# Optimization experiments

Hardware: AMD Instinct MI355X
Metric: run time of the kernel (lower is better)

## Reference

```python
import jax, jax.numpy as jnp
import numpy as np

NEG_BIG = -9e15
ALPHA = 0.2  # LeakyReLU negative slope


def setup_inputs() -> dict:
    key = jax.random.key(0)
    k1, k2, k3, k4 = jax.random.split(key, 4)
    N, Fin, Fout = 8192, 256, 256
    input_ = jax.random.normal(k1, (N, Fin), dtype=jnp.float32)
    adj = jax.random.randint(k2, (N, N), 0, 2, dtype=jnp.int32)
    # xavier_uniform with gain=1.414
    limW = 1.414 * np.sqrt(6.0 / (Fin + Fout))
    W = jax.random.uniform(k3, (Fin, Fout), minval=-limW, maxval=limW, dtype=jnp.float32)
    lima = 1.414 * np.sqrt(6.0 / (2 * Fout + 1))
    a = jax.random.uniform(k4, (2 * Fout, 1), minval=-lima, maxval=lima, dtype=jnp.float32)
    return {"input_": input_, "adj": adj, "W": W, "a": a}


def reference(input_, adj, W, a):
    # h: [N, F]
    h = input_ @ W
    F = h.shape[1]
    # Decompose cat([h_i, h_j]) @ a into per-node projections summed by broadcast
    src = h @ a[:F, 0]   # [N]  contribution of row node i
    dst = h @ a[F:, 0]   # [N]  contribution of col node j
    e = jax.nn.leaky_relu(src[:, None] + dst[None, :], negative_slope=ALPHA)  # [N, N]
    e = jnp.where(adj > 0, e, NEG_BIG)
    attention = jax.nn.softmax(e, axis=1)
    h_prime = attention @ h  # [N, F]
    return jax.nn.relu(h_prime)  # concat=True
```

## Files before the change

kernel.cpp:

```cpp
#include <hip/hip_runtime.h>
#include <math.h>

#define NN 8192
#define FF 256
#define ALPHA 0.2f
#define SS 8
#define JSEG (NN / SS)
#define STEPS (JSEG / 32)

typedef __bf16 bf16x8 __attribute__((ext_vector_type(8)));
typedef __bf16 bf16x4 __attribute__((ext_vector_type(4)));
typedef float  f32x4  __attribute__((ext_vector_type(4)));

__device__ __forceinline__ void dma16(const void* g, void* l) {
    __builtin_amdgcn_global_load_lds((const __attribute__((address_space(1))) void*)g,
                                     (__attribute__((address_space(3))) void*)l,
                                     16, 0, 0);
}

#define VMCNT0   asm volatile("s_waitcnt vmcnt(0)" ::: "memory")
#define LGKM0    asm volatile("s_waitcnt lgkmcnt(0)" ::: "memory")
#define BARRIER  asm volatile("s_barrier" ::: "memory")
#define FENCE    asm volatile("" ::: "memory")

__global__ __launch_bounds__(256) void k0_wt(const float* __restrict__ W,
                                             __bf16* __restrict__ WT) {
    __shared__ float ts[64][65];
    const int t = threadIdx.x;
    const int k0 = blockIdx.x * 64;
    const int n0 = blockIdx.y * 64;
    #pragma unroll
    for (int r = 0; r < 4; ++r) {
        int krow = r * 16 + (t >> 4);
        int nc4 = (t & 15) * 4;
        *(float4*)&ts[krow][nc4] = *(const float4*)&W[(size_t)(k0 + krow) * FF + n0 + nc4];
    }
    __syncthreads();
    const int nloc = t >> 2;
    const int kc = (t & 3) * 16;
    union { bf16x8 v[2]; __bf16 e[16]; } hi, lo;
    #pragma unroll
    for (int u = 0; u < 16; ++u) {
        float x = ts[kc + u][nloc];
        __bf16 h1 = (__bf16)x;
        hi.e[u] = h1;
        lo.e[u] = (__bf16)(x - (float)h1);
    }
    size_t base = (size_t)(n0 + nloc) * FF + k0 + kc;
    *(bf16x8*)&WT[base] = hi.v[0];
    *(bf16x8*)&WT[base + 8] = hi.v[1];
    size_t lbase = (size_t)FF * FF + base;
    *(bf16x8*)&WT[lbase] = lo.v[0];
    *(bf16x8*)&WT[lbase + 8] = lo.v[1];
}

__global__ __launch_bounds__(256) void k1_h(const float* __restrict__ X,
                                            const __bf16* __restrict__ WT,
                                            const float* __restrict__ a,
                                            __bf16* __restrict__ hT,
                                            float* __restrict__ src,
                                            float* __restrict__ dst) {
    __shared__ __bf16 ax[2][32][40];
    __shared__ float hs[32][264];
    __shared__ float red[2][4][32];
    const int t = threadIdx.x;
    const int i0 = blockIdx.x * 32;
    const int l = t & 63, wv = t >> 6, ln = l & 15, g = l >> 4;
    f32x4 acc[2][4];
    #pragma unroll
    for (int mt = 0; mt < 2; ++mt)
        #pragma unroll
        for (int nt = 0; nt < 4; ++nt)
            acc[mt][nt] = (f32x4){0.f, 0.f, 0.f, 0.f};

    for (int ks = 0; ks < 8; ++ks) {
        const int k0 = ks * 32;
        {
            int row = t >> 3, c4 = (t & 7) * 4;
            float4 xv = *(const float4*)&X[(size_t)(i0 + row) * FF + k0 + c4];
            bf16x4 hi4, lo4;
            float xs_[4] = {xv.x, xv.y, xv.z, xv.w};
            #pragma unroll
            for (int u = 0; u < 4; ++u) {
                __bf16 h1 = (__bf16)xs_[u];
                hi4[u] = h1;
                lo4[u] = (__bf16)(xs_[u] - (float)h1);
            }
            *(bf16x4*)&ax[0][row][c4] = hi4;
            *(bf16x4*)&ax[1][row][c4] = lo4;
        }
        __syncthreads();
        bf16x8 ah[2], al[2];
        ah[0] = *(bf16x8*)&ax[0][ln][g * 8];
        ah[1] = *(bf16x8*)&ax[0][16 + ln][g * 8];
        al[0] = *(bf16x8*)&ax[1][ln][g * 8];
        al[1] = *(bf16x8*)&ax[1][16 + ln][g * 8];
        #pragma unroll
        for (int nt = 0; nt < 4; ++nt) {
            const int n = wv * 64 + nt * 16 + ln;
            bf16x8 bh8 = *(const bf16x8*)&WT[(size_t)n * FF + k0 + g * 8];
            bf16x8 bl8 = *(const bf16x8*)&WT[(size_t)(FF + n) * FF + k0 + g * 8];
            #pragma unroll
            for (int mt = 0; mt < 2; ++mt) {
                acc[mt][nt] = __builtin_amdgcn_mfma_f32_16x16x32_bf16(ah[mt], bh8, acc[mt][nt], 0, 0, 0);
                acc[mt][nt] = __builtin_amdgcn_mfma_f32_16x16x32_bf16(ah[mt], bl8, acc[mt][nt], 0, 0, 0);
                acc[mt][nt] = __builtin_amdgcn_mfma_f32_16x16x32_bf16(al[mt], bh8, acc[mt][nt], 0, 0, 0);
            }
        }
        __syncthreads();
    }
    float an[4], ad[4];
    #pragma unroll
    for (int nt = 0; nt < 4; ++nt) {
        an[nt] = a[wv * 64 + nt * 16 + ln];
        ad[nt] = a[FF + wv * 64 + nt * 16 + ln];
    }
    float sp[2][4], dp[2][4];
    #pragma unroll
    for (int mt = 0; mt < 2; ++mt)
        #pragma unroll
        for (int rg = 0; rg < 4; ++rg) { sp[mt][rg] = 0.f; dp[mt][rg] = 0.f; }
    #pragma unroll
    for (int mt = 0; mt < 2; ++mt)
        #pragma unroll
        for (int nt = 0; nt < 4; ++nt)
            #pragma unroll
            for (int rg = 0; rg < 4; ++rg) {
                float v = acc[mt][nt][rg];
                hs[mt * 16 + g * 4 + rg][wv * 64 + nt * 16 + ln] = v;
                sp[mt][rg] += v * an[nt];
                dp[mt][rg] += v * ad[nt];
            }
    #pragma unroll
    for (int mk = 1; mk < 16; mk <<= 1)
        #pragma unroll
        for (int mt = 0; mt < 2; ++mt)
            #pragma unroll
            for (int rg = 0; rg < 4; ++rg) {
                sp[mt][rg] += __shfl_xor(sp[mt][rg], mk);
                dp[mt][rg] += __shfl_xor(dp[mt][rg], mk);
            }
    if (ln == 0) {
        #pragma unroll
        for (int mt = 0; mt < 2; ++mt)
            #pragma unroll
            for (int rg = 0; rg < 4; ++rg) {
                red[0][wv][mt * 16 + g * 4 + rg] = sp[mt][rg];
                red[1][wv][mt * 16 + g * 4 + rg] = dp[mt][rg];
            }
    }
    __syncthreads();
    if (t < 32) {
        src[i0 + t] = red[0][0][t] + red[0][1][t] + red[0][2][t] + red[0][3][t];
        dst[i0 + t] = red[1][0][t] + red[1][1][t] + red[1][2][t] + red[1][3][t];
    }
    {
        const int f = t;
        #pragma unroll
        for (int jc = 0; jc < 4; ++jc) {
            union { bf16x8 v; __bf16 e[8]; } hi;
            #pragma unroll
            for (int u = 0; u < 8; ++u) {
                float x = hs[jc * 8 + u][f];
                hi.e[u] = (__bf16)x;
            }
            *(bf16x8*)&hT[(size_t)f * NN + i0 + jc * 8] = hi.v;
        }
    }
}

__global__ __launch_bounds__(256) void k2a_pack(const int* __restrict__ adj,
                                                unsigned* __restrict__ bits) {
    const size_t total4 = (size_t)NN * NN / 4;
    const int l = threadIdx.x & 63;
    const int base = l & 56;
    size_t t = (size_t)blockIdx.x * 256 + threadIdx.x;
    const size_t stride = (size_t)gridDim.x * 256;
    for (; t < total4; t += stride) {
        int4 v = ((const int4*)adj)[t];
        unsigned nib = (unsigned)(v.x > 0) | ((unsigned)(v.y > 0) << 1)
                     | ((unsigned)(v.z > 0) << 2) | ((unsigned)(v.w > 0) << 3);
        unsigned w = 0;
        #pragma unroll
        for (int k = 0; k < 8; ++k)
            w |= (unsigned)__shfl((int)nib, base + k) << (4 * k);
        if ((l & 7) == 0)
            bits[t >> 3] = w;
    }
}

__global__ __launch_bounds__(256) void k2b_max(const float* __restrict__ dst,
                                               float* __restrict__ maxd) {
    __shared__ float red[256];
    float m = -1e30f;
    #pragma unroll
    for (int r = 0; r < NN / 1024; ++r) {
        float4 v = *(const float4*)&dst[(r * 256 + threadIdx.x) * 4];
        m = fmaxf(m, fmaxf(fmaxf(v.x, v.y), fmaxf(v.z, v.w)));
    }
    red[threadIdx.x] = m;
    __syncthreads();
    for (int s = 128; s > 0; s >>= 1) {
        if (threadIdx.x < s) red[threadIdx.x] = fmaxf(red[threadIdx.x], red[threadIdx.x + s]);
        __syncthreads();
    }
    if (threadIdx.x == 0) maxd[0] = red[0];
}

__global__ __launch_bounds__(256, 4) void k3_attn(const unsigned* __restrict__ bits,
                                                  const __bf16* __restrict__ hT,
                                                  const float* __restrict__ src,
                                                  const float* __restrict__ dst,
                                                  const float* __restrict__ maxd,
                                                  float* __restrict__ num,
                                                  float* __restrict__ den) {
    __shared__ __bf16 bh[2][1024 * 8];
    __shared__ float dsts[JSEG];
    const int t = threadIdx.x;
    const int l = t & 63, wv = t >> 6, ln = l & 15, g = l >> 4;
    const int it = blockIdx.x & 127;
    const int seg = blockIdx.x >> 7;
    const int i0 = it * 64;
    const int jbeg = seg * JSEG;
    const int rl = wv * 16 + ln;
    const int row = i0 + rl;
    const float maxdv = maxd[0];
    const float src_r = src[row];
    const float e0 = src_r + maxdv;
    const float m_r = e0 > 0.f ? e0 : ALPHA * e0;

    int ga[4], cb[4];
    #pragma unroll
    for (int r = 0; r < 4; ++r) {
        int cbase = r * 256 + wv * 64;
        int c = cbase + l;
        int f = c >> 2;
        int pc = c & 3;
        int jc = pc ^ ((f >> 1) & 3);
        ga[r] = f * NN + jc * 8;
        cb[r] = __builtin_amdgcn_readfirstlane(cbase);
    }
    const int rb = ln * 64 + ((g ^ ((ln >> 1) & 3)) * 16);
    const char* bh0 = (const char*)&bh[0][0] + rb;
    const char* bh1 = (const char*)&bh[1][0] + rb;

    const unsigned* grow = bits + (size_t)row * (NN / 32) + (jbeg >> 5);

    #pragma unroll
    for (int r = 0; r < 4; ++r)
        dma16(&hT[ga[r] + jbeg], &bh[0][cb[r] * 8]);
    FENCE;
    *(float4*)&dsts[t * 4] = *(const float4*)&dst[jbeg + t * 4];
    uint2 wp = *(const uint2*)&grow[0];
    uint2 wpn = wp;
    __syncthreads();

    float den_reg = 0.f;
    f32x4 acc[16];
    #pragma unroll
    for (int nt = 0; nt < 16; ++nt) acc[nt] = (f32x4){0.f, 0.f, 0.f, 0.f};

#define K3_WCOMP(S_, MW_, AF_)                                                \
    {                                                                         \
        unsigned mb = ((MW_) >> (g * 8)) & 0xffu;                             \
        const float* dp_ = &dsts[(S_) * 32 + g * 8];                          \
        float4 dq0 = *(const float4*)dp_;                                     \
        float4 dq1 = *(const float4*)(dp_ + 4);                               \
        const float dv[8] = {dq0.x, dq0.y, dq0.z, dq0.w,                      \
                             dq1.x, dq1.y, dq1.z, dq1.w};                     \
        _Pragma("unroll")                                                     \
        for (int u = 0; u < 8; ++u) {                                         \
            float e = src_r + dv[u];                                          \
            e = e > 0.f ? e : ALPHA * e;                                      \
            float ex = __expf(e - m_r);                                       \
            float w = (mb & (1u << u)) ? ex : 0.f;                            \
            den_reg += w;                                                     \
            AF_.e[u] = (__bf16)w;                                             \
        }                                                                     \
    }

#define K3_MFMA(AF_, BP_)                                                     \
    {                                                                         \
        _Pragma("unroll")                                                     \
        for (int nt = 0; nt < 16; ++nt) {                                     \
            bf16x8 bfr = *(const bf16x8*)((BP_) + nt * 1024);                 \
            acc[nt] = __builtin_amdgcn_mfma_f32_16x16x32_bf16(                \
                AF_.v, bfr, acc[nt], 0, 0, 0);                                \
        }                                                                     \
    }

    for (int s = 0; s < STEPS; s += 2) {
        union { bf16x8 v; __bf16 e[8]; } afe;
        K3_WCOMP(s, wp.x, afe);
        FENCE; VMCNT0; LGKM0; BARRIER;
        #pragma unroll
        for (int r = 0; r < 4; ++r)
            dma16(&hT[ga[r] + jbeg + (s + 1) * 32], &bh[1][cb[r] * 8]);
        if (s + 2 < STEPS) wpn = *(const uint2*)&grow[s + 2];
        FENCE;
        K3_MFMA(afe, bh0);
        union { bf16x8 v; __bf16 e[8]; } afo;
        K3_WCOMP(s + 1, wp.y, afo);
        FENCE; VMCNT0; LGKM0; BARRIER;
        {
            int sn = (s + 2 < STEPS) ? s + 2 : 0;
            #pragma unroll
            for (int r = 0; r < 4; ++r)
                dma16(&hT[ga[r] + jbeg + sn * 32], &bh[0][cb[r] * 8]);
        }
        FENCE;
        K3_MFMA(afo, bh1);
        wp = wpn;
    }
    den_reg += __shfl_xor(den_reg, 16);
    den_reg += __shfl_xor(den_reg, 32);
    if (g == 0) den[(size_t)seg * NN + row] = den_reg;
    #pragma unroll
    for (int nt = 0; nt < 16; ++nt)
        #pragma unroll
        for (int rg = 0; rg < 4; ++rg)
            num[((size_t)seg * NN + i0 + wv * 16 + g * 4 + rg) * FF
                + nt * 16 + ln] = acc[nt][rg];
}

__global__ __launch_bounds__(256) void k4_out(const float* __restrict__ num,
                                              const float* __restrict__ den,
                                              float* __restrict__ out) {
    size_t f4 = (size_t)blockIdx.x * 256 + threadIdx.x;
    int i = (int)(f4 >> 6);
    int c4 = (int)(f4 & 63) << 2;
    float4 s = make_float4(0.f, 0.f, 0.f, 0.f);
    float d = 0.f;
    #pragma unroll
    for (int sg = 0; sg < SS; ++sg) {
        float4 v = *(const float4*)&num[((size_t)sg * NN + i) * FF + c4];
        s.x += v.x; s.y += v.y; s.z += v.z; s.w += v.w;
        d += den[(size_t)sg * NN + i];
    }
    float inv = 1.f / d;
    float4 o;
    o.x = fmaxf(s.x * inv, 0.f);
    o.y = fmaxf(s.y * inv, 0.f);
    o.z = fmaxf(s.z * inv, 0.f);
    o.w = fmaxf(s.w * inv, 0.f);
    *(float4*)&out[(size_t)i * FF + c4] = o;
}

extern "C" void kernel_launch(void* const* d_in, const int* in_sizes, int n_in,
                              void* d_out, int out_size, void* d_ws, size_t ws_size,
                              hipStream_t stream) {
    const float* X  = (const float*)d_in[0];
    const int*  adj = (const int*)d_in[1];
    const float* W  = (const float*)d_in[2];
    const float* a  = (const float*)d_in[3];
    float* out = (float*)d_out;
    char* ws = (char*)d_ws;

    const size_t off_hT   = 0;
    const size_t off_wt   = off_hT + (size_t)FF * NN * 2;
    const size_t off_src  = off_wt + (size_t)2 * FF * FF * 2;
    const size_t off_dst  = off_src + (size_t)NN * 4;
    const size_t off_maxd = off_dst + (size_t)NN * 4;
    const size_t off_num  = off_maxd + 256;
    const size_t off_den  = off_num + (size_t)SS * NN * FF * 4;
    const size_t off_bits = off_den + (size_t)SS * NN * 4;

    __bf16* hT_ws = (__bf16*)(ws + off_hT);
    __bf16* wt_ws = (__bf16*)(ws + off_wt);
    float* src_ws = (float*)(ws + off_src);
    float* dst_ws = (float*)(ws + off_dst);
    float* maxd   = (float*)(ws + off_maxd);
    float* num_ws = (float*)(ws + off_num);
    float* den_ws = (float*)(ws + off_den);
    unsigned* bits_ws = (unsigned*)(ws + off_bits);

    k2a_pack<<<2048, 256, 0, stream>>>(adj, bits_ws);
    k0_wt<<<dim3(FF / 64, FF / 64), 256, 0, stream>>>(W, wt_ws);
    k1_h<<<NN / 32, 256, 0, stream>>>(X, wt_ws, a, hT_ws, src_ws, dst_ws);
    k2b_max<<<1, 256, 0, stream>>>(dst_ws, maxd);
    k3_attn<<<(NN / 64) * SS, 256, 0, stream>>>(bits_ws, hT_ws, src_ws, dst_ws, maxd,
                                                num_ws, den_ws);
    k4_out<<<(NN * FF / 4) / 256, 256, 0, stream>>>(num_ws, den_ws, out);
}
```

Baseline: 455.4 us.

## Switch attention kernel to 32x32x16 MFMA with 128-row tiles

After: 456.0 us. About the same (+0.1%).

```diff
diff --git a/kernel.cpp b/kernel.cpp
--- a/kernel.cpp
+++ b/kernel.cpp
@@ -7,10 +7,12 @@
 #define SS 8
 #define JSEG (NN / SS)
 #define STEPS (JSEG / 32)
+#define BI 128
 
 typedef __bf16 bf16x8 __attribute__((ext_vector_type(8)));
 typedef __bf16 bf16x4 __attribute__((ext_vector_type(4)));
 typedef float  f32x4  __attribute__((ext_vector_type(4)));
+typedef float  f32x16 __attribute__((ext_vector_type(16)));
 
 __device__ __forceinline__ void dma16(const void* g, void* l) {
     __builtin_amdgcn_global_load_lds((const __attribute__((address_space(1))) void*)g,
@@ -207,7 +209,7 @@
     if (threadIdx.x == 0) maxd[0] = red[0];
 }
 
-__global__ __launch_bounds__(256, 4) void k3_attn(const unsigned* __restrict__ bits,
+__global__ __launch_bounds__(256, 2) void k3_attn(const unsigned* __restrict__ bits,
                                                   const __bf16* __restrict__ hT,
                                                   const float* __restrict__ src,
                                                   const float* __restrict__ dst,
@@ -217,13 +219,13 @@
     __shared__ __bf16 bh[2][1024 * 8];
     __shared__ float dsts[JSEG];
     const int t = threadIdx.x;
-    const int l = t & 63, wv = t >> 6, ln = l & 15, g = l >> 4;
-    const int it = blockIdx.x & 127;
-    const int seg = blockIdx.x >> 7;
-    const int i0 = it * 64;
+    const int l = t & 63, wv = t >> 6;
+    const int q = l & 31, hi = l >> 5;
+    const int it = blockIdx.x & 63;
+    const int seg = blockIdx.x >> 6;
+    const int i0 = it * BI;
     const int jbeg = seg * JSEG;
-    const int rl = wv * 16 + ln;
-    const int row = i0 + rl;
+    const int row = i0 + wv * 32 + q;
     const float maxdv = maxd[0];
     const float src_r = src[row];
     const float e0 = src_r + maxdv;
@@ -236,13 +238,14 @@
         int c = cbase + l;
         int f = c >> 2;
         int pc = c & 3;
-        int jc = pc ^ ((f >> 1) & 3);
+        int jc = pc ^ (f & 3);
         ga[r] = f * NN + jc * 8;
         cb[r] = __builtin_amdgcn_readfirstlane(cbase);
     }
-    const int rb = ln * 64 + ((g ^ ((ln >> 1) & 3)) * 16);
-    const char* bh0 = (const char*)&bh[0][0] + rb;
-    const char* bh1 = (const char*)&bh[1][0] + rb;
+    const int rb0 = q * 64 + (((0 + hi) ^ (q & 3)) * 16);
+    const int rb1 = q * 64 + (((2 + hi) ^ (q & 3)) * 16);
+    const char* bh0 = (const char*)&bh[0][0];
+    const char* bh1 = (const char*)&bh[1][0];
 
     const unsigned* grow = bits + (size_t)row * (NN / 32) + (jbeg >> 5);
 
@@ -256,51 +259,68 @@
     __syncthreads();
 
     float den_reg = 0.f;
-    f32x4 acc[16];
-    #pragma unroll
-    for (int nt = 0; nt < 16; ++nt) acc[nt] = (f32x4){0.f, 0.f, 0.f, 0.f};
-
-#define K3_WCOMP(S_, MW_, AF_)                                                \
+    f32x16 acc[8];
+    #pragma unroll
+    for (int ft = 0; ft < 8; ++ft)
+        #pragma unroll
+        for (int rg = 0; rg < 16; ++rg) acc[ft][rg] = 0.f;
+
+#define K3_WCOMP(S_, MW_, AF0_, AF1_)                                         \
     {                                                                         \
-        unsigned mb = ((MW_) >> (g * 8)) & 0xffu;                             \
-        const float* dp_ = &dsts[(S_) * 32 + g * 8];                          \
-        float4 dq0 = *(const float4*)dp_;                                     \
-        float4 dq1 = *(const float4*)(dp_ + 4);                               \
-        const float dv[8] = {dq0.x, dq0.y, dq0.z, dq0.w,                      \
-                             dq1.x, dq1.y, dq1.z, dq1.w};                     \
+        unsigned mb0 = ((MW_) >> (hi * 8)) & 0xffu;                           \
+        unsigned mb1 = ((MW_) >> (16 + hi * 8)) & 0xffu;                      \
+        const float* dp0 = &dsts[(S_) * 32 + hi * 8];                         \
+        float4 a0 = *(const float4*)dp0;                                      \
+        float4 a1 = *(const float4*)(dp0 + 4);                                \
+        float4 b0 = *(const float4*)(dp0 + 16);                               \
+        float4 b1 = *(const float4*)(dp0 + 20);                               \
+        const float dv0[8] = {a0.x, a0.y, a0.z, a0.w, a1.x, a1.y, a1.z, a1.w};\
+        const float dv1[8] = {b0.x, b0.y, b0.z, b0.w, b1.x, b1.y, b1.z, b1.w};\
         _Pragma("unroll")                                                     \
         for (int u = 0; u < 8; ++u) {                                         \
-            float e = src_r + dv[u];                                          \
+            float e = src_r + dv0[u];                                         \
             e = e > 0.f ? e : ALPHA * e;                                      \
             float ex = __expf(e - m_r);                                       \
-            float w = (mb & (1u << u)) ? ex : 0.f;                            \
+            float w = (mb0 & (1u << u)) ? ex : 0.f;                           \
             den_reg += w;                                                     \
-            AF_.e[u] = (__bf16)w;                                             \
+            AF0_.e[u] = (__bf16)w;                                            \
         }                                                                     \
-    }
-
-#define K3_MFMA(AF_, BP_)                                                     \
+        _Pragma("unroll")                                                     \
+        for (int u = 0; u < 8; ++u) {                                         \
+            float e = src_r + dv1[u];                                         \
+            e = e > 0.f ? e : ALPHA * e;                                      \
+            float ex = __expf(e - m_r);                                       \
+            float w = (mb1 & (1u << u)) ? ex : 0.f;                           \
+            den_reg += w;                                                     \
+            AF1_.e[u] = (__bf16)w;                                            \
+        }                                                                     \
+    }
+
+#define K3_MFMA(AF0_, AF1_, BP_)                                              \
     {                                                                         \
         _Pragma("unroll")                                                     \
-        for (int nt = 0; nt < 16; ++nt) {                                     \
-            bf16x8 bfr = *(const bf16x8*)((BP_) + nt * 1024);                 \
-            acc[nt] = __builtin_amdgcn_mfma_f32_16x16x32_bf16(                \
-                AF_.v, bfr, acc[nt], 0, 0, 0);                                \
+        for (int ft = 0; ft < 8; ++ft) {                                      \
+            bf16x8 bk0 = *(const bf16x8*)((BP_) + ft * 2048 + rb0);           \
+            bf16x8 bk1 = *(const bf16x8*)((BP_) + ft * 2048 + rb1);           \
+            acc[ft] = __builtin_amdgcn_mfma_f32_32x32x16_bf16(                \
+                AF0_.v, bk0, acc[ft], 0, 0, 0);                               \
+            acc[ft] = __builtin_amdgcn_mfma_f32_32x32x16_bf16(                \
+                AF1_.v, bk1, acc[ft], 0, 0, 0);                               \
         }                                                                     \
     }
 
     for (int s = 0; s < STEPS; s += 2) {
-        union { bf16x8 v; __bf16 e[8]; } afe;
-        K3_WCOMP(s, wp.x, afe);
+        union { bf16x8 v; __bf16 e[8]; } af0e, af1e;
+        K3_WCOMP(s, wp.x, af0e, af1e);
         FENCE; VMCNT0; LGKM0; BARRIER;
         #pragma unroll
         for (int r = 0; r < 4; ++r)
             dma16(&hT[ga[r] + jbeg + (s + 1) * 32], &bh[1][cb[r] * 8]);
         if (s + 2 < STEPS) wpn = *(const uint2*)&grow[s + 2];
         FENCE;
-        K3_MFMA(afe, bh0);
-        union { bf16x8 v; __bf16 e[8]; } afo;
-        K3_WCOMP(s + 1, wp.y, afo);
+        K3_MFMA(af0e, af1e, bh0);
+        union { bf16x8 v; __bf16 e[8]; } af0o, af1o;
+        K3_WCOMP(s + 1, wp.y, af0o, af1o);
         FENCE; VMCNT0; LGKM0; BARRIER;
         {
             int sn = (s + 2 < STEPS) ? s + 2 : 0;
@@ -309,18 +329,18 @@
                 dma16(&hT[ga[r] + jbeg + sn * 32], &bh[0][cb[r] * 8]);
         }
         FENCE;
-        K3_MFMA(afo, bh1);
+        K3_MFMA(af0o, af1o, bh1);
         wp = wpn;
     }
-    den_reg += __shfl_xor(den_reg, 16);
     den_reg += __shfl_xor(den_reg, 32);
-    if (g == 0) den[(size_t)seg * NN + row] = den_reg;
-    #pragma unroll
-    for (int nt = 0; nt < 16; ++nt)
-        #pragma unroll
-        for (int rg = 0; rg < 4; ++rg)
-            num[((size_t)seg * NN + i0 + wv * 16 + g * 4 + rg) * FF
-                + nt * 16 + ln] = acc[nt][rg];
+    if (hi == 0) den[(size_t)seg * NN + row] = den_reg;
+    #pragma unroll
+    for (int ft = 0; ft < 8; ++ft)
+        #pragma unroll
+        for (int rg = 0; rg < 16; ++rg) {
+            int m = (rg & 3) + 8 * (rg >> 2) + 4 * hi;
+            num[((size_t)seg * NN + i0 + wv * 32 + m) * FF + ft * 32 + q] = acc[ft][rg];
+        }
 }
 
 __global__ __launch_bounds__(256) void k4_out(const float* __restrict__ num,
@@ -378,7 +398,7 @@
     k0_wt<<<dim3(FF / 64, FF / 64), 256, 0, stream>>>(W, wt_ws);
     k1_h<<<NN / 32, 256, 0, stream>>>(X, wt_ws, a, hT_ws, src_ws, dst_ws);
     k2b_max<<<1, 256, 0, stream>>>(dst_ws, maxd);
-    k3_attn<<<(NN / 64) * SS, 256, 0, stream>>>(bits_ws, hT_ws, src_ws, dst_ws, maxd,
+    k3_attn<<<(NN / BI) * SS, 256, 0, stream>>>(bits_ws, hT_ws, src_ws, dst_ws, maxd,
                                                 num_ws, den_ws);
     k4_out<<<(NN * FF / 4) / 256, 256, 0, stream>>>(num_ws, den_ws, out);
 }
```
